# Performance work log

Measured on AMD Instinct MI355X. Metric: run time of the kernel, lower is better.

## Reference

```python
import jax, jax.numpy as jnp
import numpy as np

N_DIM = 128
M_SEQ = 2048
BATCH = 256


def setup_inputs() -> dict:
    key = jax.random.key(0)
    k1, k2, k3 = jax.random.split(key, 3)
    scale = 1.0 / np.sqrt(N_DIM)
    return {
        "x": jax.random.normal(k1, (BATCH, N_DIM, M_SEQ), dtype=jnp.float32),
        "W": jax.random.normal(k2, (N_DIM, 3 * N_DIM), dtype=jnp.float32) * scale,
        "U": jax.random.normal(k3, (N_DIM, 3 * N_DIM), dtype=jnp.float32) * scale,
        "b": jnp.zeros((3 * N_DIM,), dtype=jnp.float32),
    }


def reference(x, W, U, b):
    # x: [B, D, T] -> scan over T with a GRU cell, output [B, D, T]
    B, D, T = x.shape
    xs = jnp.transpose(x, (2, 0, 1))  # [T, B, D]

    def cell(h, xt):
        gx = xt @ W + b              # [B, 3D]
        gh = h @ U                   # [B, 3D]
        xz, xr, xn = jnp.split(gx, 3, axis=-1)
        hz, hr, hn = jnp.split(gh, 3, axis=-1)
        z = jax.nn.sigmoid(xz + hz)  # update gate
        r = jax.nn.sigmoid(xr + hr)  # reset gate
        n = jnp.tanh(xn + r * hn)    # candidate
        h_new = z * h + (1.0 - z) * n
        return h_new, h_new

    h0 = jnp.zeros((B, D), dtype=x.dtype)
    _, ys = jax.lax.scan(cell, h0, xs)   # ys: [T, B, D]
    return jnp.transpose(ys, (1, 2, 0))  # [B, D, T]
```

## Files before the change

### kernel.cpp

```cpp
#include <hip/hip_runtime.h>

typedef float f32x4 __attribute__((ext_vector_type(4)));
typedef short bf16x8 __attribute__((ext_vector_type(8)));

#define TT    2048
#define DDIM  128
#define G3    384
#define NBBLK 16
#define GXROW 6144
#define GX_BYTES ((size_t)NBBLK * TT * GXROW * 2)

__device__ __forceinline__ unsigned f2bf_u(float f) {
    unsigned u = __float_as_uint(f);
    return (u + 0x7FFFu + ((u >> 16) & 1u)) >> 16;
}
__device__ __forceinline__ float bf_lo(unsigned u) { return __uint_as_float(u << 16); }
__device__ __forceinline__ float bf_hi(unsigned u) { return __uint_as_float(u & 0xffff0000u); }
__device__ __forceinline__ float rcp_(float x) { return __builtin_amdgcn_rcpf(x); }
__device__ __forceinline__ float sigm_(float v) { return rcp_(1.0f + __expf(-v)); }
__device__ __forceinline__ float tanhf_(float v) { return 2.0f * rcp_(1.0f + __expf(-2.0f * v)) - 1.0f; }
__device__ __forceinline__ unsigned cvt_pk_bf16(float lo, float hi) {
    unsigned d;
    asm("v_cvt_pk_bf16_f32 %0, %1, %2" : "=v"(d) : "v"(lo), "v"(hi));
    return d;
}

__global__ __launch_bounds__(256) void gx_gemm(
    const float* __restrict__ x, const float* __restrict__ W,
    const float* __restrict__ bias, unsigned short* __restrict__ gx)
{
    const int bblk  = blockIdx.x;
    const int ttile = blockIdx.y;
    const int tid = threadIdx.x;
    const int w  = tid >> 6;
    const int l  = tid & 63;
    const int lc = l & 15;
    const int lk = l >> 4;

    __shared__ unsigned short xs[16 * 16 * DDIM];

    const int tiles[6] = {2*w, 2*w+1, 2*w+8, 2*w+9, 2*w+16, 2*w+17};

    bf16x8 wfrag[6][4];
    f32x4  binit[6];
    #pragma unroll
    for (int i6 = 0; i6 < 6; ++i6) {
        const int c = tiles[i6] * 16 + lc;
        const float bv = bias[c];
        binit[i6] = (f32x4){bv, bv, bv, bv};
        #pragma unroll
        for (int kt = 0; kt < 4; ++kt) {
            bf16x8 f;
            #pragma unroll
            for (int jj = 0; jj < 8; ++jj) {
                const int k = kt * 32 + lk * 8 + jj;
                f[jj] = (short)f2bf_u(W[k * G3 + c]);
            }
            wfrag[i6][kt] = f;
        }
    }

    int inoff[4];
    #pragma unroll
    for (int kt = 0; kt < 4; ++kt)
        inoff[kt] = (lc * 256 + kt * 64 + lk * 16) ^ ((lc & 7) << 4);

    const float* xb = x + (size_t)bblk * 16 * DDIM * TT;
    const int t0blk = ttile * 128;
    const int tq = tid & 3;
    const int pbase = tid >> 2;

    for (int chunk = 0; chunk < 8; ++chunk) {
        __syncthreads();
        const int t0 = t0blk + chunk * 16 + tq * 4;
        #pragma unroll 4
        for (int pp = 0; pp < 32; ++pp) {
            const int p = pbase + pp * 64;
            const int r = p >> 7, d = p & 127;
            f32x4 v = *(const f32x4*)(xb + (size_t)p * TT + t0);
            char* bp = (char*)xs + (tq * 4) * 4096 + (((r * 128 + d) * 2) ^ ((r & 7) << 4));
            const unsigned pkA = cvt_pk_bf16(v[0], v[1]);
            const unsigned pkB = cvt_pk_bf16(v[2], v[3]);
            *(unsigned short*)(bp)         = (unsigned short)pkA;
            *(unsigned short*)(bp + 4096)  = (unsigned short)(pkA >> 16);
            *(unsigned short*)(bp + 8192)  = (unsigned short)pkB;
            *(unsigned short*)(bp + 12288) = (unsigned short)(pkB >> 16);
        }
        __syncthreads();

        for (int t = 0; t < 16; ++t) {
            bf16x8 a[4];
            #pragma unroll
            for (int kt = 0; kt < 4; ++kt)
                a[kt] = *(const bf16x8*)((const char*)xs + t * 4096 + inoff[kt]);

            const int tglob = t0blk + chunk * 16 + t;
            #pragma unroll
            for (int i6 = 0; i6 < 6; ++i6) {
                f32x4 acc = binit[i6];
                #pragma unroll
                for (int kt = 0; kt < 4; ++kt)
                    acc = __builtin_amdgcn_mfma_f32_16x16x32_bf16(a[kt], wfrag[i6][kt], acc, 0, 0, 0);
                unsigned p0 = cvt_pk_bf16(acc[0], acc[1]);
                unsigned p1 = cvt_pk_bf16(acc[2], acc[3]);
                const int tt6 = tiles[i6];
                const int cb = tt6 & 7, g = tt6 >> 3;
                const size_t off = ((size_t)(bblk * TT + tglob) * 8 + cb) * 768
                                   + g * 256 + l * 4;
                *(uint2*)(gx + off) = make_uint2(p0, p1);
            }
        }
    }
}

__global__ __launch_bounds__(512, 2) void gru_rec(
    const unsigned short* __restrict__ gx, const float* __restrict__ U,
    float* __restrict__ out)
{
    const int bblk = blockIdx.x;
    const int tid  = threadIdx.x;
    const int w  = tid >> 6;
    const int l  = tid & 63;
    const int lc = l & 15, lk = l >> 4;
    const int c  = w * 16 + lc;

    bf16x8 uz[4], ur[4], un[4];
    #pragma unroll
    for (int kt = 0; kt < 4; ++kt) {
        bf16x8 fz, fr, fn;
        #pragma unroll
        for (int jj = 0; jj < 8; ++jj) {
            const int k = kt * 32 + lk * 8 + jj;
            fz[jj] = (short)f2bf_u(U[k * G3 + c]);
            fr[jj] = (short)f2bf_u(U[k * G3 + 128 + c]);
            fn[jj] = (short)f2bf_u(U[k * G3 + 256 + c]);
        }
        uz[kt] = fz; ur[kt] = fr; un[kt] = fn;
    }

    __shared__ unsigned short hsA[2 * 2048];
    __shared__ float hlds[16 * 16 * 128];
    #pragma unroll
    for (int i = tid; i < 4096; i += 512) hsA[i] = 0;
    char* const hb_lds = (char*)hlds;

    int roff[4];
    #pragma unroll
    for (int kt = 0; kt < 4; ++kt)
        roff[kt] = (lc * 256 + kt * 64 + lk * 16) ^ ((lc & 7) << 4);

    unsigned widxB[4];
    #pragma unroll
    for (int i = 0; i < 4; ++i) {
        const int r = lk * 4 + i;
        widxB[i] = (unsigned)(((r * 128 + c) ^ ((r & 7) << 3)) * 2);
    }

    int hl_addr[4][4];
    #pragma unroll
    for (int s = 0; s < 4; ++s)
        #pragma unroll
        for (int i = 0; i < 4; ++i) {
            const int r = lk * 4 + i;
            hl_addr[s][i] = s * 32768 + (r * 128 + ((c + 8 * lk + 8 * s) & 127)) * 4;
        }

    const int cfl = w * 16 + (l >> 2);
    const int qfl = l & 3;
    int fl_base[4];
    #pragma unroll
    for (int g = 0; g < 4; ++g)
        fl_base[g] = qfl * 32768 + ((cfl + 8 * g + 8 * qfl) & 127) * 4;

    float hold[4] = {0.f, 0.f, 0.f, 0.f};

    const unsigned short* g0 = gx + ((size_t)bblk * TT * 8 + w) * 768 + l * 4;
    float* outb = out + (size_t)(bblk * 16) * DDIM * TT;

    uint2 rgz[4], rgr[4], rgn[4];
    #pragma unroll
    for (int d = 0; d < 4; ++d) {
        const unsigned short* gq = g0 + (size_t)d * GXROW;
        rgz[d] = *(const uint2*)(gq);
        rgr[d] = *(const uint2*)(gq + 256);
        rgn[d] = *(const uint2*)(gq + 512);
    }

    __syncthreads();

#define GATE(I, J)                                                            \
    {                                                                         \
        const float zz = sigm_(az_a[I] + az_b[I]);                            \
        const float rr = sigm_(ar_a[I] + ar_b[I]);                            \
        const float uu = gn##I + rr * (an_a[I] + an_b[I]);                    \
        const float nn = tanhf_(uu);                                          \
        const float hn = nn + zz * (hold[I] - nn);                            \
        hold[I] = hn;                                                         \
        *(float*)(hb_lds + hl_addr[(J) >> 2][I] + ((J) & 3) * 8192) = hn;     \
        hh[I] = hn;                                                           \
    }

#define SUBSTEP(J, DOPF)                                                      \
    {                                                                         \
        const char* hb = (const char*)hsA + ((J) & 1) * 4096;                 \
        bf16x8 a0 = *(const bf16x8*)(hb + roff[0]);                           \
        bf16x8 a1 = *(const bf16x8*)(hb + roff[1]);                           \
        bf16x8 a2 = *(const bf16x8*)(hb + roff[2]);                           \
        bf16x8 a3 = *(const bf16x8*)(hb + roff[3]);                           \
        uint2 pz = rgz[(J) & 3], pr = rgr[(J) & 3], pn = rgn[(J) & 3];        \
        if (DOPF) {                                                           \
            const unsigned short* gq = gpt + (size_t)((J) + 4) * GXROW;       \
            rgz[(J) & 3] = *(const uint2*)(gq);                               \
            rgr[(J) & 3] = *(const uint2*)(gq + 256);                         \
            rgn[(J) & 3] = *(const uint2*)(gq + 512);                         \
        }                                                                     \
        f32x4 az_a, ar_a;                                                     \
        az_a[0] = bf_lo(pz.x); az_a[1] = bf_hi(pz.x);                         \
        az_a[2] = bf_lo(pz.y); az_a[3] = bf_hi(pz.y);                         \
        ar_a[0] = bf_lo(pr.x); ar_a[1] = bf_hi(pr.x);                         \
        ar_a[2] = bf_lo(pr.y); ar_a[3] = bf_hi(pr.y);                         \
        const float gn0 = bf_lo(pn.x), gn1 = bf_hi(pn.x);                     \
        const float gn2 = bf_lo(pn.y), gn3 = bf_hi(pn.y);                     \
        f32x4 an_a = (f32x4){0.f, 0.f, 0.f, 0.f};                             \
        f32x4 an_b = an_a, az_b = an_a, ar_b = an_a;                          \
        an_a = __builtin_amdgcn_mfma_f32_16x16x32_bf16(a0, un[0], an_a, 0, 0, 0); \
        an_b = __builtin_amdgcn_mfma_f32_16x16x32_bf16(a2, un[2], an_b, 0, 0, 0); \
        az_a = __builtin_amdgcn_mfma_f32_16x16x32_bf16(a0, uz[0], az_a, 0, 0, 0); \
        az_b = __builtin_amdgcn_mfma_f32_16x16x32_bf16(a2, uz[2], az_b, 0, 0, 0); \
        ar_a = __builtin_amdgcn_mfma_f32_16x16x32_bf16(a0, ur[0], ar_a, 0, 0, 0); \
        ar_b = __builtin_amdgcn_mfma_f32_16x16x32_bf16(a2, ur[2], ar_b, 0, 0, 0); \
        an_a = __builtin_amdgcn_mfma_f32_16x16x32_bf16(a1, un[1], an_a, 0, 0, 0); \
        an_b = __builtin_amdgcn_mfma_f32_16x16x32_bf16(a3, un[3], an_b, 0, 0, 0); \
        az_a = __builtin_amdgcn_mfma_f32_16x16x32_bf16(a1, uz[1], az_a, 0, 0, 0); \
        az_b = __builtin_amdgcn_mfma_f32_16x16x32_bf16(a3, uz[3], az_b, 0, 0, 0); \
        ar_a = __builtin_amdgcn_mfma_f32_16x16x32_bf16(a1, ur[1], ar_a, 0, 0, 0); \
        ar_b = __builtin_amdgcn_mfma_f32_16x16x32_bf16(a3, ur[3], ar_b, 0, 0, 0); \
        float hh[4];                                                          \
        GATE(0, J) GATE(1, J) GATE(2, J) GATE(3, J)                           \
        {                                                                     \
            char* hwb = (char*)hsA + (((J) & 1) ^ 1) * 4096;                  \
            const unsigned pk01 = cvt_pk_bf16(hh[0], hh[1]);                  \
            const unsigned pk23 = cvt_pk_bf16(hh[2], hh[3]);                  \
            *(unsigned short*)(hwb + widxB[0]) = (unsigned short)pk01;        \
            *(unsigned short*)(hwb + widxB[1]) = (unsigned short)(pk01 >> 16);\
            *(unsigned short*)(hwb + widxB[2]) = (unsigned short)pk23;        \
            *(unsigned short*)(hwb + widxB[3]) = (unsigned short)(pk23 >> 16);\
        }                                                                     \
        asm volatile("s_waitcnt lgkmcnt(0)" ::: "memory");                    \
        __builtin_amdgcn_s_barrier();                                         \
    }

#define FLUSH(T0)                                                             \
    _Pragma("unroll")                                                         \
    for (int r = 0; r < 16; ++r) {                                            \
        f32x4 v;                                                              \
        _Pragma("unroll")                                                     \
        for (int k = 0; k < 4; ++k)                                           \
            v[k] = *(const float*)(hb_lds + fl_base[r >> 2] + r * 512 + k * 8192); \
        *(f32x4*)(outb + ((size_t)r * DDIM + cfl) * TT + (T0) + qfl * 4) = v; \
    }

    for (int t = 0; t < TT - 16; t += 16) {
        const unsigned short* gpt = g0 + (size_t)t * GXROW;
        SUBSTEP(0, true)  SUBSTEP(1, true)  SUBSTEP(2, true)  SUBSTEP(3, true)
        SUBSTEP(4, true)  SUBSTEP(5, true)  SUBSTEP(6, true)  SUBSTEP(7, true)
        SUBSTEP(8, true)  SUBSTEP(9, true)  SUBSTEP(10, true) SUBSTEP(11, true)
        SUBSTEP(12, true) SUBSTEP(13, true) SUBSTEP(14, true) SUBSTEP(15, true)
        FLUSH(t)
    }
    {
        const int t = TT - 16;
        const unsigned short* gpt = g0 + (size_t)t * GXROW;
        SUBSTEP(0, true)  SUBSTEP(1, true)  SUBSTEP(2, true)  SUBSTEP(3, true)
        SUBSTEP(4, true)  SUBSTEP(5, true)  SUBSTEP(6, true)  SUBSTEP(7, true)
        SUBSTEP(8, true)  SUBSTEP(9, true)  SUBSTEP(10, true) SUBSTEP(11, true)
        SUBSTEP(12, false) SUBSTEP(13, false) SUBSTEP(14, false) SUBSTEP(15, false)
        FLUSH(t)
    }
#undef GATE
#undef SUBSTEP
#undef FLUSH
}

typedef float f32x2 __attribute__((ext_vector_type(2)));

__global__ __launch_bounds__(768) void gru_fused(
    const float* __restrict__ x, const float* __restrict__ W,
    const float* __restrict__ U, const float* __restrict__ b,
    float* __restrict__ out)
{
    const int bb  = blockIdx.x;
    const int tid = threadIdx.x;
    const int kh  = (tid >= G3) ? 1 : 0;
    const int c   = tid - kh * G3;
    const int kbase = kh * 64;

    f32x2 wcol[32], ucol[32];
    #pragma unroll
    for (int k2 = 0; k2 < 32; ++k2) {
        wcol[k2][0] = W[(size_t)(kbase + 2*k2 + 0) * G3 + c];
        wcol[k2][1] = W[(size_t)(kbase + 2*k2 + 1) * G3 + c];
        ucol[k2][0] = U[(size_t)(kbase + 2*k2 + 0) * G3 + c];
        ucol[k2][1] = U[(size_t)(kbase + 2*k2 + 1) * G3 + c];
    }
    const float bias = b[c];

    __shared__ float xs[2][DDIM];
    __shared__ float hs[DDIM];
    __shared__ float px[G3], ph[G3];
    __shared__ float rs[DDIM], ns[DDIM];

    if (tid < DDIM) { hs[tid] = 0.0f; xs[0][tid] = x[((size_t)bb * DDIM + tid) * TT]; }
    __syncthreads();

    const float* __restrict__ xrow = x   + (size_t)bb * DDIM * TT;
    float* __restrict__       orow = out + (size_t)bb * DDIM * TT;
    float zv = 0.0f;

    for (int t = 0; t < TT; ++t) {
        const float* xcur = xs[t & 1] + kbase;
        const float* hcur = hs + kbase;
        f32x2 axv = {0.f, 0.f}, ahv = {0.f, 0.f};
        #pragma unroll
        for (int k2 = 0; k2 < 32; ++k2) {
            f32x2 xv = *(const f32x2*)(xcur + 2*k2);
            f32x2 hv = *(const f32x2*)(hcur + 2*k2);
            axv += xv * wcol[k2];
            ahv += hv * ucol[k2];
        }
        float ax = axv[0] + axv[1];
        float ah = ahv[0] + ahv[1];
        if (kh) { px[c] = ax; ph[c] = ah; }
        if (t + 1 < TT && tid >= 128 && tid < 256) {
            const int k = tid - 128;
            xs[(t + 1) & 1][k] = xrow[(size_t)k * TT + (t + 1)];
        }
        __syncthreads();
        if (!kh) {
            ax += px[c]; ah += ph[c];
            if (c < DDIM)            zv = sigm_(ax + ah + bias);
            else if (c < 2*DDIM)     rs[c - DDIM] = sigm_(ax + ah + bias);
            else { px[c] = ax + bias; ph[c] = ah; }
        }
        __syncthreads();
        if (!kh && c >= 2*DDIM) {
            float r = rs[c - 2*DDIM];
            ns[c - 2*DDIM] = tanhf_(px[c] + r * ph[c]);
        }
        __syncthreads();
        if (tid < DDIM) {
            float n = ns[tid];
            float hnew = zv * hs[tid] + (1.0f - zv) * n;
            hs[tid] = hnew;
            orow[(size_t)tid * TT + t] = hnew;
        }
        __syncthreads();
    }
}

extern "C" void kernel_launch(void* const* d_in, const int* in_sizes, int n_in,
                              void* d_out, int out_size, void* d_ws, size_t ws_size,
                              hipStream_t stream) {
    const float* x = (const float*)d_in[0];
    const float* W = (const float*)d_in[1];
    const float* U = (const float*)d_in[2];
    const float* b = (const float*)d_in[3];
    float* out     = (float*)d_out;

    if (ws_size >= GX_BYTES) {
        unsigned short* gx = (unsigned short*)d_ws;
        hipLaunchKernelGGL(gx_gemm, dim3(16, 16), dim3(256), 0, stream, x, W, b, gx);
        hipLaunchKernelGGL(gru_rec, dim3(16), dim3(512), 0, stream, gx, U, out);
    } else {
        hipLaunchKernelGGL(gru_fused, dim3(256), dim3(768), 0, stream, x, W, U, b, out);
    }
}
```

Baseline: 1.797 ms.

## Transpose MFMA operands, fold exp2 scaling into weights, vectorize LDS stores

Swaps the MFMA operand order so each lane holds 4 consecutive feature columns, not 4 batch rows. This lets the recurrent kernel write h to LDS with one packed 8-byte store and one 16-byte f32x4 store per step instead of scattered 2-byte and 4-byte stores. Gate pre-activation weights and bias are pre-scaled by -log2(e) and -2*log2(e) so the gates use raw v_exp_f32 without a per-element multiply. The gx layout and the XOR swizzles for LDS and flush are redone to match. Scaling before the bf16 rounding slightly changes numerics.

```diff
diff --git a/kernel.cpp b/kernel.cpp
--- a/kernel.cpp
+++ b/kernel.cpp
@@ -10,6 +10,9 @@
 #define GXROW 6144
 #define GX_BYTES ((size_t)NBBLK * TT * GXROW * 2)
 
+#define SCL_ZR (-1.4426950408889634f)
+#define SCL_N  (-2.8853900817779268f)
+
 __device__ __forceinline__ unsigned f2bf_u(float f) {
     unsigned u = __float_as_uint(f);
     return (u + 0x7FFFu + ((u >> 16) & 1u)) >> 16;
@@ -17,8 +20,13 @@
 __device__ __forceinline__ float bf_lo(unsigned u) { return __uint_as_float(u << 16); }
 __device__ __forceinline__ float bf_hi(unsigned u) { return __uint_as_float(u & 0xffff0000u); }
 __device__ __forceinline__ float rcp_(float x) { return __builtin_amdgcn_rcpf(x); }
-__device__ __forceinline__ float sigm_(float v) { return rcp_(1.0f + __expf(-v)); }
-__device__ __forceinline__ float tanhf_(float v) { return 2.0f * rcp_(1.0f + __expf(-2.0f * v)) - 1.0f; }
+__device__ __forceinline__ float exp2_(float x) {
+    float d;
+    asm("v_exp_f32 %0, %1" : "=v"(d) : "v"(x));
+    return d;
+}
+__device__ __forceinline__ float sigm_(float v) { return rcp_(1.0f + exp2_(-1.4426950408889634f * v)); }
+__device__ __forceinline__ float tanhf_(float v) { return 2.0f * rcp_(1.0f + exp2_(-2.8853900817779268f * v)) - 1.0f; }
 __device__ __forceinline__ unsigned cvt_pk_bf16(float lo, float hi) {
     unsigned d;
     asm("v_cvt_pk_bf16_f32 %0, %1, %2" : "=v"(d) : "v"(lo), "v"(hi));
@@ -45,16 +53,17 @@
     f32x4  binit[6];
     #pragma unroll
     for (int i6 = 0; i6 < 6; ++i6) {
-        const int c = tiles[i6] * 16 + lc;
-        const float bv = bias[c];
-        binit[i6] = (f32x4){bv, bv, bv, bv};
+        const float scl = (i6 >= 4) ? SCL_N : SCL_ZR;
+        #pragma unroll
+        for (int i = 0; i < 4; ++i)
+            binit[i6][i] = bias[tiles[i6] * 16 + lk * 4 + i] * scl;
         #pragma unroll
         for (int kt = 0; kt < 4; ++kt) {
             bf16x8 f;
             #pragma unroll
             for (int jj = 0; jj < 8; ++jj) {
                 const int k = kt * 32 + lk * 8 + jj;
-                f[jj] = (short)f2bf_u(W[k * G3 + c]);
+                f[jj] = (short)f2bf_u(W[k * G3 + tiles[i6] * 16 + lc] * scl);
             }
             wfrag[i6][kt] = f;
         }
@@ -100,13 +109,11 @@
                 f32x4 acc = binit[i6];
                 #pragma unroll
                 for (int kt = 0; kt < 4; ++kt)
-                    acc = __builtin_amdgcn_mfma_f32_16x16x32_bf16(a[kt], wfrag[i6][kt], acc, 0, 0, 0);
+                    acc = __builtin_amdgcn_mfma_f32_16x16x32_bf16(wfrag[i6][kt], a[kt], acc, 0, 0, 0);
                 unsigned p0 = cvt_pk_bf16(acc[0], acc[1]);
                 unsigned p1 = cvt_pk_bf16(acc[2], acc[3]);
-                const int tt6 = tiles[i6];
-                const int cb = tt6 & 7, g = tt6 >> 3;
-                const size_t off = ((size_t)(bblk * TT + tglob) * 8 + cb) * 768
-                                   + g * 256 + l * 4;
+                const size_t off = (size_t)(bblk * TT + tglob) * GXROW
+                                   + (size_t)(((tiles[i6] * 4 + lk) * 16 + lc) * 4);
                 *(uint2*)(gx + off) = make_uint2(p0, p1);
             }
         }
@@ -122,7 +129,6 @@
     const int w  = tid >> 6;
     const int l  = tid & 63;
     const int lc = l & 15, lk = l >> 4;
-    const int c  = w * 16 + lc;
 
     bf16x8 uz[4], ur[4], un[4];
     #pragma unroll
@@ -131,9 +137,9 @@
         #pragma unroll
         for (int jj = 0; jj < 8; ++jj) {
             const int k = kt * 32 + lk * 8 + jj;
-            fz[jj] = (short)f2bf_u(U[k * G3 + c]);
-            fr[jj] = (short)f2bf_u(U[k * G3 + 128 + c]);
-            fn[jj] = (short)f2bf_u(U[k * G3 + 256 + c]);
+            fz[jj] = (short)f2bf_u(U[k * G3 + (w * 16 + lc)] * SCL_ZR);
+            fr[jj] = (short)f2bf_u(U[k * G3 + 128 + (w * 16 + lc)] * SCL_ZR);
+            fn[jj] = (short)f2bf_u(U[k * G3 + 256 + (w * 16 + lc)] * SCL_N);
         }
         uz[kt] = fz; ur[kt] = fr; un[kt] = fn;
     }
@@ -147,72 +153,62 @@
     int roff[4];
     #pragma unroll
     for (int kt = 0; kt < 4; ++kt)
-        roff[kt] = (lc * 256 + kt * 64 + lk * 16) ^ ((lc & 7) << 4);
-
-    unsigned widxB[4];
-    #pragma unroll
-    for (int i = 0; i < 4; ++i) {
-        const int r = lk * 4 + i;
-        widxB[i] = (unsigned)(((r * 128 + c) ^ ((r & 7) << 3)) * 2);
-    }
-
-    int hl_addr[4][4];
-    #pragma unroll
-    for (int s = 0; s < 4; ++s)
-        #pragma unroll
-        for (int i = 0; i < 4; ++i) {
-            const int r = lk * 4 + i;
-            hl_addr[s][i] = s * 32768 + (r * 128 + ((c + 8 * lk + 8 * s) & 127)) * 4;
-        }
-
-    const int cfl = w * 16 + (l >> 2);
+        roff[kt] = lc * 256 + ((kt * 64 + lk * 16) ^ (lc << 4));
+
+    const int wb64 = lc * 256 + ((w * 32 + lk * 8) ^ (lc << 4));
+
+    int hlv[4];
+    {
+        const int hlbase = lc * 512 + ((w * 64 + lk * 16) ^ ((lc & 7) << 4));
+        #pragma unroll
+        for (int s = 0; s < 4; ++s) hlv[s] = hlbase ^ (s << 6);
+    }
+
+    const int dl  = w * 16 + (l >> 2);
     const int qfl = l & 3;
-    int fl_base[4];
-    #pragma unroll
-    for (int g = 0; g < 4; ++g)
-        fl_base[g] = qfl * 32768 + ((cfl + 8 * g + 8 * qfl) & 127) * 4;
+    const int flb = qfl * 32768 + ((dl * 4) ^ (qfl << 6));
+    float* outl = out + ((size_t)bblk * 16 * DDIM + dl) * TT + qfl * 4;
 
     float hold[4] = {0.f, 0.f, 0.f, 0.f};
 
-    const unsigned short* g0 = gx + ((size_t)bblk * TT * 8 + w) * 768 + l * 4;
-    float* outb = out + (size_t)(bblk * 16) * DDIM * TT;
+    const unsigned short* g0 = gx + (size_t)bblk * TT * GXROW
+                               + (size_t)(((w * 4 + lk) * 16 + lc) * 4);
 
     uint2 rgz[4], rgr[4], rgn[4];
     #pragma unroll
     for (int d = 0; d < 4; ++d) {
         const unsigned short* gq = g0 + (size_t)d * GXROW;
         rgz[d] = *(const uint2*)(gq);
-        rgr[d] = *(const uint2*)(gq + 256);
-        rgn[d] = *(const uint2*)(gq + 512);
+        rgr[d] = *(const uint2*)(gq + 2048);
+        rgn[d] = *(const uint2*)(gq + 4096);
     }
 
     __syncthreads();
 
-#define GATE(I, J)                                                            \
+#define GATE(I)                                                               \
     {                                                                         \
-        const float zz = sigm_(az_a[I] + az_b[I]);                            \
-        const float rr = sigm_(ar_a[I] + ar_b[I]);                            \
+        const float zz = rcp_(1.0f + exp2_(az_a[I] + az_b[I]));               \
+        const float rr = rcp_(1.0f + exp2_(ar_a[I] + ar_b[I]));               \
         const float uu = gn##I + rr * (an_a[I] + an_b[I]);                    \
-        const float nn = tanhf_(uu);                                          \
+        const float nn = 2.0f * rcp_(1.0f + exp2_(uu)) - 1.0f;                \
         const float hn = nn + zz * (hold[I] - nn);                            \
         hold[I] = hn;                                                         \
-        *(float*)(hb_lds + hl_addr[(J) >> 2][I] + ((J) & 3) * 8192) = hn;     \
         hh[I] = hn;                                                           \
     }
 
 #define SUBSTEP(J, DOPF)                                                      \
     {                                                                         \
         const char* hb = (const char*)hsA + ((J) & 1) * 4096;                 \
-        bf16x8 a0 = *(const bf16x8*)(hb + roff[0]);                           \
-        bf16x8 a1 = *(const bf16x8*)(hb + roff[1]);                           \
-        bf16x8 a2 = *(const bf16x8*)(hb + roff[2]);                           \
-        bf16x8 a3 = *(const bf16x8*)(hb + roff[3]);                           \
+        bf16x8 b0 = *(const bf16x8*)(hb + roff[0]);                           \
+        bf16x8 b1 = *(const bf16x8*)(hb + roff[1]);                           \
+        bf16x8 b2 = *(const bf16x8*)(hb + roff[2]);                           \
+        bf16x8 b3 = *(const bf16x8*)(hb + roff[3]);                           \
         uint2 pz = rgz[(J) & 3], pr = rgr[(J) & 3], pn = rgn[(J) & 3];        \
         if (DOPF) {                                                           \
             const unsigned short* gq = gpt + (size_t)((J) + 4) * GXROW;       \
             rgz[(J) & 3] = *(const uint2*)(gq);                               \
-            rgr[(J) & 3] = *(const uint2*)(gq + 256);                         \
-            rgn[(J) & 3] = *(const uint2*)(gq + 512);                         \
+            rgr[(J) & 3] = *(const uint2*)(gq + 2048);                        \
+            rgn[(J) & 3] = *(const uint2*)(gq + 4096);                        \
         }                                                                     \
         f32x4 az_a, ar_a;                                                     \
         az_a[0] = bf_lo(pz.x); az_a[1] = bf_hi(pz.x);                         \
@@ -223,29 +219,28 @@
         const float gn2 = bf_lo(pn.y), gn3 = bf_hi(pn.y);                     \
         f32x4 an_a = (f32x4){0.f, 0.f, 0.f, 0.f};                             \
         f32x4 an_b = an_a, az_b = an_a, ar_b = an_a;                          \
-        an_a = __builtin_amdgcn_mfma_f32_16x16x32_bf16(a0, un[0], an_a, 0, 0, 0); \
-        an_b = __builtin_amdgcn_mfma_f32_16x16x32_bf16(a2, un[2], an_b, 0, 0, 0); \
-        az_a = __builtin_amdgcn_mfma_f32_16x16x32_bf16(a0, uz[0], az_a, 0, 0, 0); \
-        az_b = __builtin_amdgcn_mfma_f32_16x16x32_bf16(a2, uz[2], az_b, 0, 0, 0); \
-        ar_a = __builtin_amdgcn_mfma_f32_16x16x32_bf16(a0, ur[0], ar_a, 0, 0, 0); \
-        ar_b = __builtin_amdgcn_mfma_f32_16x16x32_bf16(a2, ur[2], ar_b, 0, 0, 0); \
-        an_a = __builtin_amdgcn_mfma_f32_16x16x32_bf16(a1, un[1], an_a, 0, 0, 0); \
-        an_b = __builtin_amdgcn_mfma_f32_16x16x32_bf16(a3, un[3], an_b, 0, 0, 0); \
-        az_a = __builtin_amdgcn_mfma_f32_16x16x32_bf16(a1, uz[1], az_a, 0, 0, 0); \
-        az_b = __builtin_amdgcn_mfma_f32_16x16x32_bf16(a3, uz[3], az_b, 0, 0, 0); \
-        ar_a = __builtin_amdgcn_mfma_f32_16x16x32_bf16(a1, ur[1], ar_a, 0, 0, 0); \
-        ar_b = __builtin_amdgcn_mfma_f32_16x16x32_bf16(a3, ur[3], ar_b, 0, 0, 0); \
+        an_a = __builtin_amdgcn_mfma_f32_16x16x32_bf16(un[0], b0, an_a, 0, 0, 0); \
+        an_b = __builtin_amdgcn_mfma_f32_16x16x32_bf16(un[2], b2, an_b, 0, 0, 0); \
+        az_a = __builtin_amdgcn_mfma_f32_16x16x32_bf16(uz[0], b0, az_a, 0, 0, 0); \
+        az_b = __builtin_amdgcn_mfma_f32_16x16x32_bf16(uz[2], b2, az_b, 0, 0, 0); \
+        ar_a = __builtin_amdgcn_mfma_f32_16x16x32_bf16(ur[0], b0, ar_a, 0, 0, 0); \
+        ar_b = __builtin_amdgcn_mfma_f32_16x16x32_bf16(ur[2], b2, ar_b, 0, 0, 0); \
+        an_a = __builtin_amdgcn_mfma_f32_16x16x32_bf16(un[1], b1, an_a, 0, 0, 0); \
+        an_b = __builtin_amdgcn_mfma_f32_16x16x32_bf16(un[3], b3, an_b, 0, 0, 0); \
+        az_a = __builtin_amdgcn_mfma_f32_16x16x32_bf16(uz[1], b1, az_a, 0, 0, 0); \
+        az_b = __builtin_amdgcn_mfma_f32_16x16x32_bf16(uz[3], b3, az_b, 0, 0, 0); \
+        ar_a = __builtin_amdgcn_mfma_f32_16x16x32_bf16(ur[1], b1, ar_a, 0, 0, 0); \
+        ar_b = __builtin_amdgcn_mfma_f32_16x16x32_bf16(ur[3], b3, ar_b, 0, 0, 0); \
         float hh[4];                                                          \
-        GATE(0, J) GATE(1, J) GATE(2, J) GATE(3, J)                           \
+        GATE(0) GATE(1) GATE(2) GATE(3)                                       \
         {                                                                     \
-            char* hwb = (char*)hsA + (((J) & 1) ^ 1) * 4096;                  \
             const unsigned pk01 = cvt_pk_bf16(hh[0], hh[1]);                  \
             const unsigned pk23 = cvt_pk_bf16(hh[2], hh[3]);                  \
-            *(unsigned short*)(hwb + widxB[0]) = (unsigned short)pk01;        \
-            *(unsigned short*)(hwb + widxB[1]) = (unsigned short)(pk01 >> 16);\
-            *(unsigned short*)(hwb + widxB[2]) = (unsigned short)pk23;        \
-            *(unsigned short*)(hwb + widxB[3]) = (unsigned short)(pk23 >> 16);\
+            *(uint2*)((char*)hsA + ((((J) & 1) ^ 1) * 4096) + wb64)           \
+                = make_uint2(pk01, pk23);                                     \
         }                                                                     \
+        *(f32x4*)(hb_lds + hlv[(J) >> 2] + (J) * 8192)                        \
+            = (f32x4){hh[0], hh[1], hh[2], hh[3]};                            \
         asm volatile("s_waitcnt lgkmcnt(0)" ::: "memory");                    \
         __builtin_amdgcn_s_barrier();                                         \
     }
@@ -253,11 +248,12 @@
 #define FLUSH(T0)                                                             \
     _Pragma("unroll")                                                         \
     for (int r = 0; r < 16; ++r) {                                            \
+        const int fr = (flb ^ ((r & 7) << 4)) + r * 512;                      \
         f32x4 v;                                                              \
         _Pragma("unroll")                                                     \
         for (int k = 0; k < 4; ++k)                                           \
-            v[k] = *(const float*)(hb_lds + fl_base[r >> 2] + r * 512 + k * 8192); \
-        *(f32x4*)(outb + ((size_t)r * DDIM + cfl) * TT + (T0) + qfl * 4) = v; \
+            v[k] = *(const float*)(hb_lds + fr + k * 8192);                   \
+        *(f32x4*)(outl + (size_t)r * (DDIM * TT) + (T0)) = v;                 \
     }
 
     for (int t = 0; t < TT - 16; t += 16) {
```

After: 1.676 ms. -6.7%, faster.
